# Kernel optimization log

Measured on AMD Instinct MI355X. Metric: run time of the kernel, lower is better.

The kernel has to match this reference:

```python
import jax, jax.numpy as jnp
import numpy as np


def _forward(f2e_emb, score_mat, rel_features, Wk, bk,
             batch_heads, batch_rels, batch_tails, edge_mat, eps):
    B, N, D = f2e_emb.shape
    R = rel_features.shape[0]
    dt = f2e_emb.dtype
    # -cdist(x, x) then row softmax (F.softmax dim=1 on a 2D mat == last axis)
    x2 = jnp.sum(f2e_emb * f2e_emb, axis=-1)                              # [B,N]
    d2 = x2[:, :, None] + x2[:, None, :] - 2.0 * jnp.einsum('bnd,bmd->bnm', f2e_emb, f2e_emb)
    sim = jax.nn.softmax(-jnp.sqrt(jnp.maximum(d2, 0.0)), axis=-1)        # [B,N,N]
    prob = jnp.einsum('bnk,bmk->bnm', sim, score_mat)                     # sim @ score_mat.T
    cand = (prob > eps) & (edge_mat < 1)                                  # candidate (row,col) pairs
    # torch.multinomial(sim[row], 1) per candidate pair -> gumbel-max categorical,
    # one independent draw per (b, row, col) over the row's similarity distribution
    logits = jnp.log(sim)[:, :, None, :]                                  # [B,N,1,N]
    s = jax.random.categorical(jax.random.key(42),
                               jax.lax.stop_gradient(jnp.broadcast_to(logits, (B, N, N, N))),
                               axis=-1)                                    # [B,N,N]
    b3 = jnp.arange(B)[:, None, None]
    r3 = jnp.arange(N)[None, :, None]
    c3 = jnp.arange(N)[None, None, :]
    new_rel = edge_mat[b3, s, c3]                                          # [B,N,N]
    valid = (cand & (new_rel != 0)).astype(dt)
    # per-(node, relation) incidence counts: exactly equivalent to the
    # fact2head_mat/fact2tail_mat sparse.mm aggregation of kb_self_linear(rel_features[rel])
    counts = jnp.zeros((B * N * R,), dt)
    counts = counts.at[((b3 * N + r3) * R + new_rel).ravel()].add(valid.ravel())  # new edge -> head
    counts = counts.at[((b3 * N + c3) * R + new_rel).ravel()].add(valid.ravel())  # new edge -> tail
    b2 = jnp.arange(B)[:, None]
    ones = jnp.ones(batch_heads.shape, dt)
    counts = counts.at[((b2 * N + batch_heads) * R + batch_rels).ravel()].add(ones.ravel())
    counts = counts.at[((b2 * N + batch_tails) * R + batch_rels).ravel()].add(ones.ravel())
    counts = counts.reshape(B, N, R)
    Wr = rel_features @ Wk + bk                                            # kb_self_linear(rel_features) [R,O]
    return jax.nn.relu(jnp.einsum('bnr,ro->bno', counts, Wr))              # [B,N,O]


def setup_inputs():
    key = jax.random.key(0)
    ks = jax.random.split(key, 10)
    B, N, D, O, R, E = 8, 256, 256, 256, 512, 8192
    return {
        'f2e_emb': jax.random.normal(ks[0], (B, N, D), jnp.float32),
        'score_mat': jax.random.normal(ks[1], (B, N, N), jnp.float32),
        'rel_features': jax.random.normal(ks[2], (R, D), jnp.float32),
        'Wk': jax.random.normal(ks[3], (D, O), jnp.float32) / np.sqrt(D).astype(np.float32),
        'bk': jnp.zeros((O,), jnp.float32),
        'local_entity': jax.random.randint(ks[4], (B, N), 0, N, jnp.int32),
        'batch_heads': jax.random.randint(ks[5], (B, E), 0, N, jnp.int32),
        'batch_rels': jax.random.randint(ks[6], (B, E), 0, R, jnp.int32),
        'batch_tails': jax.random.randint(ks[7], (B, E), 0, N, jnp.int32),
        'edge_mat': jax.random.randint(ks[8], (B, N, N), 0, 4, jnp.int32),
        'eps': 0,
    }


def reference(f2e_emb, score_mat, rel_features, Wk, bk, local_entity,
              batch_heads, batch_rels, batch_tails, edge_mat, eps):
    return _forward(f2e_emb, score_mat, rel_features, Wk, bk,
                    batch_heads, batch_rels, batch_tails, edge_mat, eps)
```

## Files before the change

kernel.cpp:

```cpp
#include <hip/hip_runtime.h>
#include <stdint.h>

#define B 8
#define N 256
#define D 256
#define O 256
#define R 512
#define E 8192
#define TRO 4
#define NSW 8192
#define F32_TINY 1.17549435e-38f

__device__ __forceinline__ void threefry2x32_k42(uint32_t x0, uint32_t x1,
                                                 uint32_t& o0, uint32_t& o1) {
  const uint32_t ks0 = 0u;
  const uint32_t ks1 = 42u;
  const uint32_t ks2 = 0u ^ 42u ^ 0x1BD11BDAu;
  x0 += ks0; x1 += ks1;
#define TF_R(r) { x0 += x1; x1 = (x1 << (r)) | (x1 >> (32 - (r))); x1 ^= x0; }
  TF_R(13) TF_R(15) TF_R(26) TF_R(6)
  x0 += ks1; x1 += ks2 + 1u;
  TF_R(17) TF_R(29) TF_R(16) TF_R(24)
  x0 += ks2; x1 += ks0 + 2u;
  TF_R(13) TF_R(15) TF_R(26) TF_R(6)
  x0 += ks0; x1 += ks1 + 3u;
  TF_R(17) TF_R(29) TF_R(16) TF_R(24)
  x0 += ks1; x1 += ks2 + 4u;
  TF_R(13) TF_R(15) TF_R(26) TF_R(6)
  x0 += ks2; x1 += ks0 + 5u;
#undef TF_R
  o0 = x0; o1 = x1;
}

__device__ __forceinline__ float gumbel_from_bits_f(float f) {
  float u = (f == 0.0f) ? F32_TINY : f;
  return -logf(-logf(u));
}

__global__ __launch_bounds__(256) void prep_kernel(const float* __restrict__ score,
                                                   float* __restrict__ scoreT,
                                                   const float* __restrict__ f2e,
                                                   float* __restrict__ f2eT,
                                                   const float* __restrict__ relf,
                                                   const float* __restrict__ Wk,
                                                   const float* __restrict__ bk,
                                                   float* __restrict__ Wr,
                                                   float* __restrict__ x2,
                                                   int* __restrict__ wcount) {
  int blk = blockIdx.x;
  int tid = threadIdx.x;
  if (blk == 0 && tid == 0) *wcount = 0;
  if (blk < 256) {
    __shared__ float tile[64][65];
    const float* src = (blk < 128) ? score : f2e;
    float* dst = (blk < 128) ? scoreT : f2eT;
    int b7 = blk & 127;
    int bb = b7 >> 4, t = b7 & 15, ti = t >> 2, tj = t & 3;
    size_t base = (size_t)bb * 65536;
    int c = tid & 63, r4 = tid >> 6;
#pragma unroll
    for (int rr = 0; rr < 64; rr += 4) {
      int row = rr + r4;
      tile[row][c] = src[base + (size_t)(ti * 64 + row) * 256 + tj * 64 + c];
    }
    __syncthreads();
#pragma unroll
    for (int rr = 0; rr < 64; rr += 4) {
      int row = rr + r4;
      dst[base + (size_t)(tj * 64 + row) * 256 + ti * 64 + c] = tile[c][row];
    }
  } else if (blk < 512) {
    __shared__ float rrow[2][D];
    int r0 = (blk - 256) * 2;
    int o = tid;
#pragma unroll
    for (int r = 0; r < 2; ++r) rrow[r][o] = relf[(size_t)(r0 + r) * D + o];
    __syncthreads();
    float aA0 = 0.f, aB0 = 0.f, aA1 = 0.f, aB1 = 0.f;
    for (int d = 0; d < D; d += 4) {
      float w0 = Wk[(size_t)(d + 0) * O + o];
      float w1 = Wk[(size_t)(d + 1) * O + o];
      float w2 = Wk[(size_t)(d + 2) * O + o];
      float w3 = Wk[(size_t)(d + 3) * O + o];
      float4 a0 = *(const float4*)&rrow[0][d];
      float4 a1 = *(const float4*)&rrow[1][d];
      aA0 += a0.x * w0; aB0 += a0.y * w1; aA0 += a0.z * w2; aB0 += a0.w * w3;
      aA1 += a1.x * w0; aB1 += a1.y * w1; aA1 += a1.z * w2; aB1 += a1.w * w3;
    }
    float bv = bk[o];
    Wr[(size_t)r0 * O + o] = (aA0 + aB0) + bv;
    Wr[(size_t)(r0 + 1) * O + o] = (aA1 + aB1) + bv;
  } else {
    int i = (blk - 512) * 256 + tid;
    const float4* p = (const float4*)(f2e + (size_t)i * D);
    double s = 0.0;
    for (int d = 0; d < D / 4; ++d) {
      float4 v = p[d];
      s += (double)v.x * v.x; s += (double)v.y * v.y;
      s += (double)v.z * v.z; s += (double)v.w * v.w;
    }
    x2[i] = (float)s;
  }
}

__global__ __launch_bounds__(256) void simcand_kernel(const float* __restrict__ f2e,
                                                      const float* __restrict__ f2eT,
                                                      const float* __restrict__ x2,
                                                      const float* __restrict__ scoreT,
                                                      const int* __restrict__ edge,
                                                      const int* __restrict__ epsp,
                                                      float* __restrict__ logits,
                                                      float* __restrict__ laux,
                                                      int* __restrict__ wlist,
                                                      int* __restrict__ wcount) {
  int bn0 = blockIdx.x * 2;
  int b = bn0 >> 8;
  int tid = threadIdx.x, lane = tid & 63, w = tid >> 6;
  __shared__ float arow[2][256];
  __shared__ float simrow[2][256];
  __shared__ float wred[2][4];
  __shared__ double dred[2][4];
  __shared__ float lnsh[2];
  arow[0][tid] = f2e[(size_t)bn0 * 256 + tid];
  arow[1][tid] = f2e[(size_t)(bn0 + 1) * 256 + tid];
  __syncthreads();
  float aA0 = 0.f, aB0 = 0.f, aA1 = 0.f, aB1 = 0.f;
  const float* fT = f2eT + (size_t)b * 65536 + tid;
  for (int dd = 0; dd < 256; dd += 4) {
    float b0 = fT[(size_t)(dd + 0) * 256];
    float b1 = fT[(size_t)(dd + 1) * 256];
    float b2 = fT[(size_t)(dd + 2) * 256];
    float b3 = fT[(size_t)(dd + 3) * 256];
    float4 a0 = *(const float4*)&arow[0][dd];
    float4 a1 = *(const float4*)&arow[1][dd];
    aA0 += a0.x * b0; aB0 += a0.y * b1; aA0 += a0.z * b2; aB0 += a0.w * b3;
    aA1 += a1.x * b0; aB1 += a1.y * b1; aA1 += a1.z * b2; aB1 += a1.w * b3;
  }
  float x2c = x2[b * 256 + tid];
  float neg0 = -sqrtf(fmaxf((x2[bn0] + x2c) - 2.0f * (aA0 + aB0), 0.0f));
  float neg1 = -sqrtf(fmaxf((x2[bn0 + 1] + x2c) - 2.0f * (aA1 + aB1), 0.0f));
  float m0 = neg0, m1 = neg1;
#pragma unroll
  for (int off = 32; off > 0; off >>= 1) {
    m0 = fmaxf(m0, __shfl_xor(m0, off));
    m1 = fmaxf(m1, __shfl_xor(m1, off));
  }
  if (lane == 0) { wred[0][w] = m0; wred[1][w] = m1; }
  __syncthreads();
  float mx0 = fmaxf(fmaxf(wred[0][0], wred[0][1]), fmaxf(wred[0][2], wred[0][3]));
  float mx1 = fmaxf(fmaxf(wred[1][0], wred[1][1]), fmaxf(wred[1][2], wred[1][3]));
  float p0 = expf(neg0 - mx0), p1 = expf(neg1 - mx1);
  double s0 = (double)p0, s1 = (double)p1;
#pragma unroll
  for (int off = 32; off > 0; off >>= 1) {
    s0 += __shfl_xor(s0, off);
    s1 += __shfl_xor(s1, off);
  }
  if (lane == 0) { dred[0][w] = s0; dred[1][w] = s1; }
  __syncthreads();
  float den0 = (float)(dred[0][0] + dred[0][1] + dred[0][2] + dred[0][3]);
  float den1 = (float)(dred[1][0] + dred[1][1] + dred[1][2] + dred[1][3]);
  float sv0 = p0 / den0, sv1 = p1 / den1;
  simrow[0][tid] = sv0; simrow[1][tid] = sv1;
  float l0 = logf(sv0), l1 = logf(sv1);
  logits[(size_t)bn0 * 256 + tid] = l0;
  logits[(size_t)(bn0 + 1) * 256 + tid] = l1;
  int d0 = bn0 & 255, d1 = (bn0 + 1) & 255;
  if (tid == d0) lnsh[0] = l0;
  if (tid == d1) lnsh[1] = l1;
  float e0 = (tid == d0) ? -3.4e38f : l0;
  float e1 = (tid == d1) ? -3.4e38f : l1;
#pragma unroll
  for (int off = 32; off > 0; off >>= 1) {
    e0 = fmaxf(e0, __shfl_xor(e0, off));
    e1 = fmaxf(e1, __shfl_xor(e1, off));
  }
  if (lane == 0) { wred[0][w] = e0; wred[1][w] = e1; }
  __syncthreads();
  if (tid == 0) {
    laux[2 * bn0 + 0] = lnsh[0];
    laux[2 * bn0 + 1] = fmaxf(fmaxf(wred[0][0], wred[0][1]), fmaxf(wred[0][2], wred[0][3]));
    laux[2 * bn0 + 2] = lnsh[1];
    laux[2 * bn0 + 3] = fmaxf(fmaxf(wred[1][0], wred[1][1]), fmaxf(wred[1][2], wred[1][3]));
  }
  float pA0 = 0.f, pB0 = 0.f, pA1 = 0.f, pB1 = 0.f;
  const float* sT = scoreT + (size_t)b * 65536 + tid;
  for (int kk = 0; kk < 256; kk += 4) {
    float b0 = sT[(size_t)(kk + 0) * 256];
    float b1 = sT[(size_t)(kk + 1) * 256];
    float b2 = sT[(size_t)(kk + 2) * 256];
    float b3 = sT[(size_t)(kk + 3) * 256];
    float4 q0 = *(const float4*)&simrow[0][kk];
    float4 q1 = *(const float4*)&simrow[1][kk];
    pA0 += q0.x * b0; pB0 += q0.y * b1; pA0 += q0.z * b2; pB0 += q0.w * b3;
    pA1 += q1.x * b0; pB1 += q1.y * b1; pA1 += q1.z * b2; pB1 += q1.w * b3;
  }
  float epsv = (float)epsp[0];
  float pr[2] = {pA0 + pB0, pA1 + pB1};
#pragma unroll
  for (int r = 0; r < 2; ++r) {
    int row = (bn0 + r) * 256 + tid;
    int em = edge[(size_t)row];
    bool active = (pr[r] > epsv) && (em < 1);
    unsigned long long mask = __ballot(active);
    int cnt = __popcll(mask);
    int basev = 0;
    if (lane == 0 && cnt) basev = atomicAdd(wcount, cnt);
    basev = __shfl(basev, 0);
    if (active) {
      int pos = basev + __popcll(mask & ((1ull << lane) - 1ull));
      wlist[pos] = row;
    }
  }
}

__global__ __launch_bounds__(256) void sample_kernel(const float* __restrict__ logits,
                                                     const float* __restrict__ laux,
                                                     const int* __restrict__ wlist,
                                                     const int* __restrict__ wcount,
                                                     const int* __restrict__ edge,
                                                     const int* __restrict__ heads,
                                                     const int* __restrict__ rels,
                                                     const int* __restrict__ tails,
                                                     float* __restrict__ counts) {
  int blk = blockIdx.x;
  if (blk >= 2048) {
    int i = (blk - 2048) * 256 + threadIdx.x;
    int b = i >> 13;
    int h = heads[i], r = rels[i], t = tails[i];
    atomicAdd(&counts[(size_t)(b * N + h) * R + r], 1.0f);
    atomicAdd(&counts[(size_t)(b * N + t) * R + r], 1.0f);
    return;
  }
  int lane = threadIdx.x & 63;
  int gw = blk * 4 + (threadIdx.x >> 6);
  int cnt = *wcount;
  for (int idx = gw; idx < cnt; idx += NSW) {
    int row = wlist[idx];
    int b = row >> 16;
    int n = (row >> 8) & 255;
    int c = row & 255;
    uint32_t base = (uint32_t)row << 8;
    float u0, u1, u2, u3;
    {
      uint32_t a0, a1;
#define GEN_U(q, dst)                                                     \
      threefry2x32_k42(0u, base + (uint32_t)((q) * 64 + lane), a0, a1);    \
      dst = __uint_as_float((((a0 ^ a1) >> 9)) | 0x3f800000u) - 1.0f;
      GEN_U(0, u0) GEN_U(1, u1) GEN_U(2, u2) GEN_U(3, u3)
#undef GEN_U
    }
    float l_n  = laux[2 * ((b << 8) + n) + 0];
    float Lmax = laux[2 * ((b << 8) + n) + 1];
    int qo = n >> 6;
    float uo = (qo == 0) ? u0 : (qo == 1) ? u1 : (qo == 2) ? u2 : u3;
    float u_n = __shfl(uo, n & 63);
    float v_n = gumbel_from_bits_f(u_n) + l_n;
    float thr_g = (v_n - Lmax) - 0.125f;
    float u_thr = expf(-expf(-thr_g));
    bool owner = (lane == (n & 63));
    bool anyc = ((u0 > u_thr) && !(owner && qo == 0)) |
                ((u1 > u_thr) && !(owner && qo == 1)) |
                ((u2 > u_thr) && !(owner && qo == 2)) |
                ((u3 > u_thr) && !(owner && qo == 3));
    if (!__any(anyc)) continue;

    const float* lrow = logits + (size_t)((b << 8) + n) * N;
    float bestv = -1e30f;
    int besti = 0;
    for (int q = 0; q < 4; ++q) {
      int k = q * 64 + lane;
      uint32_t o0, o1;
      threefry2x32_k42(0u, base + (uint32_t)k, o0, o1);
      uint32_t bits = o0 ^ o1;
      float f = __uint_as_float((bits >> 9) | 0x3f800000u) - 1.0f;
      float g = gumbel_from_bits_f(f);
      float v = g + lrow[k];
      if (v > bestv || (v == bestv && k < besti)) { bestv = v; besti = k; }
    }
    for (int off = 32; off > 0; off >>= 1) {
      float ov = __shfl_down(bestv, off);
      int oi = __shfl_down(besti, off);
      if (ov > bestv || (ov == bestv && oi < besti)) { bestv = ov; besti = oi; }
    }
    if (lane == 0) {
      int nr = edge[(size_t)((b << 8) + besti) * N + c];
      if (nr != 0) {
        atomicAdd(&counts[(size_t)((b << 8) + n) * R + nr], 1.0f);
        atomicAdd(&counts[(size_t)((b << 8) + c) * R + nr], 1.0f);
      }
    }
  }
}

__global__ __launch_bounds__(256) void out_kernel(const float* __restrict__ counts,
                                                  const float* __restrict__ Wr,
                                                  float* __restrict__ out) {
  int bn0 = blockIdx.x * TRO;
  int o = threadIdx.x;
  __shared__ float crow[TRO][R];
#pragma unroll
  for (int r = 0; r < TRO; ++r) {
    crow[r][o] = counts[(size_t)(bn0 + r) * R + o];
    crow[r][o + 256] = counts[(size_t)(bn0 + r) * R + 256 + o];
  }
  __syncthreads();
  float accA[TRO] = {0, 0, 0, 0}, accB[TRO] = {0, 0, 0, 0};
  for (int k = 0; k < R; k += 4) {
    float w0 = Wr[(size_t)(k + 0) * O + o];
    float w1 = Wr[(size_t)(k + 1) * O + o];
    float w2 = Wr[(size_t)(k + 2) * O + o];
    float w3 = Wr[(size_t)(k + 3) * O + o];
#pragma unroll
    for (int r = 0; r < TRO; ++r) {
      float4 cv = *(const float4*)&crow[r][k];
      accA[r] += cv.x * w0; accB[r] += cv.y * w1;
      accA[r] += cv.z * w2; accB[r] += cv.w * w3;
    }
  }
#pragma unroll
  for (int r = 0; r < TRO; ++r)
    out[(size_t)(bn0 + r) * O + o] = fmaxf(accA[r] + accB[r], 0.0f);
}

extern "C" void kernel_launch(void* const* d_in, const int* in_sizes, int n_in,
                              void* d_out, int out_size, void* d_ws, size_t ws_size,
                              hipStream_t stream) {
  (void)in_sizes; (void)n_in; (void)out_size; (void)ws_size;
  const float* f2e   = (const float*)d_in[0];
  const float* score = (const float*)d_in[1];
  const float* relf  = (const float*)d_in[2];
  const float* Wk    = (const float*)d_in[3];
  const float* bk    = (const float*)d_in[4];
  const int* heads   = (const int*)d_in[6];
  const int* rels    = (const int*)d_in[7];
  const int* tails   = (const int*)d_in[8];
  const int* edge    = (const int*)d_in[9];
  const int* epsp    = (const int*)d_in[10];
  float* out = (float*)d_out;

  float* ws     = (float*)d_ws;
  float* logits = ws;
  float* Wr     = logits + 524288;
  float* counts = Wr + 131072;
  float* scoreT = counts;
  float* f2eT   = counts + 524288;
  float* laux   = counts + 1048576;
  float* x2     = laux + 4096;
  int*   wlist  = (int*)(x2 + 2048);
  int*   wcount = wlist + 524288;

  prep_kernel<<<520, 256, 0, stream>>>(score, scoreT, f2e, f2eT,
                                       relf, Wk, bk, Wr, x2, wcount);
  simcand_kernel<<<(B * N) / 2, 256, 0, stream>>>(f2e, f2eT, x2, scoreT, edge, epsp,
                                                  logits, laux, wlist, wcount);
  hipMemsetAsync(counts, 0, (size_t)B * N * R * sizeof(float), stream);
  sample_kernel<<<2048 + 256, 256, 0, stream>>>(logits, laux, wlist, wcount, edge,
                                                heads, rels, tails, counts);
  out_kernel<<<(B * N) / TRO, 256, 0, stream>>>(counts, Wr, out);
}
```

Measured before the change: 204.8 us.

## Stage weight panels through LDS with register-prefetched float4 loads in matvec loops

Four matrix-vector style loops (Wr projection, distance GEMV, sim@score GEMV and the output counts@Wr product) used to read the B-operand one scalar per thread straight from global memory. They now load 16-row panels with float4 global loads into registers, write them to a shared buffer, and prefetch the next panel while computing on the current one. The goal is to widen memory transactions and hide global latency behind the arithmetic. In exchange each tile step adds two barriers and 16KB of extra LDS per block, which may reduce occupancy.

Measured after the change: 210.1 us. +2.6%, slower.

```diff
diff --git a/kernel.cpp b/kernel.cpp
--- a/kernel.cpp
+++ b/kernel.cpp
@@ -7,7 +7,6 @@
 #define O 256
 #define R 512
 #define E 8192
-#define TRO 4
 #define NSW 8192
 #define F32_TINY 1.17549435e-38f
 
@@ -36,6 +35,18 @@
   float u = (f == 0.0f) ? F32_TINY : f;
   return -logf(-logf(u));
 }
+
+#define LOADT(PANEL, KK)                                                      \
+  { const float* gp_ = (PANEL) + (size_t)((KK) * 16 + srow) * 256 + scol;     \
+    st0 = *(const float4*)gp_; gp_ += 1024;                                   \
+    st1 = *(const float4*)gp_; gp_ += 1024;                                   \
+    st2 = *(const float4*)gp_; gp_ += 1024;                                   \
+    st3 = *(const float4*)gp_; }
+#define WRITET()                                                              \
+  { *(float4*)&buf[srow][scol]      = st0;                                    \
+    *(float4*)&buf[srow + 4][scol]  = st1;                                    \
+    *(float4*)&buf[srow + 8][scol]  = st2;                                    \
+    *(float4*)&buf[srow + 12][scol] = st3; }
 
 __global__ __launch_bounds__(256) void prep_kernel(const float* __restrict__ score,
                                                    float* __restrict__ scoreT,
@@ -71,25 +82,33 @@
     }
   } else if (blk < 512) {
     __shared__ float rrow[2][D];
+    __shared__ float buf[16][256];
     int r0 = (blk - 256) * 2;
-    int o = tid;
-#pragma unroll
-    for (int r = 0; r < 2; ++r) rrow[r][o] = relf[(size_t)(r0 + r) * D + o];
-    __syncthreads();
+    int srow = tid >> 6, scol = (tid & 63) * 4;
+    float4 st0, st1, st2, st3;
+    rrow[0][tid] = relf[(size_t)r0 * D + tid];
+    rrow[1][tid] = relf[(size_t)(r0 + 1) * D + tid];
     float aA0 = 0.f, aB0 = 0.f, aA1 = 0.f, aB1 = 0.f;
-    for (int d = 0; d < D; d += 4) {
-      float w0 = Wk[(size_t)(d + 0) * O + o];
-      float w1 = Wk[(size_t)(d + 1) * O + o];
-      float w2 = Wk[(size_t)(d + 2) * O + o];
-      float w3 = Wk[(size_t)(d + 3) * O + o];
-      float4 a0 = *(const float4*)&rrow[0][d];
-      float4 a1 = *(const float4*)&rrow[1][d];
-      aA0 += a0.x * w0; aB0 += a0.y * w1; aA0 += a0.z * w2; aB0 += a0.w * w3;
-      aA1 += a1.x * w0; aB1 += a1.y * w1; aA1 += a1.z * w2; aB1 += a1.w * w3;
-    }
-    float bv = bk[o];
-    Wr[(size_t)r0 * O + o] = (aA0 + aB0) + bv;
-    Wr[(size_t)(r0 + 1) * O + o] = (aA1 + aB1) + bv;
+    LOADT(Wk, 0);
+    for (int kk = 0; kk < 16; ++kk) {
+      __syncthreads();
+      WRITET();
+      __syncthreads();
+      if (kk < 15) LOADT(Wk, kk + 1);
+      int dbase = kk * 16;
+#pragma unroll
+      for (int dd = 0; dd < 16; dd += 4) {
+        float4 a0 = *(const float4*)&rrow[0][dbase + dd];
+        float4 a1 = *(const float4*)&rrow[1][dbase + dd];
+        float b0 = buf[dd + 0][tid], b1 = buf[dd + 1][tid];
+        float b2 = buf[dd + 2][tid], b3 = buf[dd + 3][tid];
+        aA0 += a0.x * b0; aB0 += a0.y * b1; aA0 += a0.z * b2; aB0 += a0.w * b3;
+        aA1 += a1.x * b0; aB1 += a1.y * b1; aA1 += a1.z * b2; aB1 += a1.w * b3;
+      }
+    }
+    float bv = bk[tid];
+    Wr[(size_t)r0 * O + tid] = (aA0 + aB0) + bv;
+    Wr[(size_t)(r0 + 1) * O + tid] = (aA1 + aB1) + bv;
   } else {
     int i = (blk - 512) * 256 + tid;
     const float4* p = (const float4*)(f2e + (size_t)i * D);
@@ -118,24 +137,35 @@
   int tid = threadIdx.x, lane = tid & 63, w = tid >> 6;
   __shared__ float arow[2][256];
   __shared__ float simrow[2][256];
+  __shared__ float buf[16][256];
   __shared__ float wred[2][4];
   __shared__ double dred[2][4];
   __shared__ float lnsh[2];
+  int srow = tid >> 6, scol = (tid & 63) * 4;
+  float4 st0, st1, st2, st3;
   arow[0][tid] = f2e[(size_t)bn0 * 256 + tid];
   arow[1][tid] = f2e[(size_t)(bn0 + 1) * 256 + tid];
-  __syncthreads();
+  const float* panelF = f2eT + (size_t)b * 65536;
   float aA0 = 0.f, aB0 = 0.f, aA1 = 0.f, aB1 = 0.f;
-  const float* fT = f2eT + (size_t)b * 65536 + tid;
-  for (int dd = 0; dd < 256; dd += 4) {
-    float b0 = fT[(size_t)(dd + 0) * 256];
-    float b1 = fT[(size_t)(dd + 1) * 256];
-    float b2 = fT[(size_t)(dd + 2) * 256];
-    float b3 = fT[(size_t)(dd + 3) * 256];
-    float4 a0 = *(const float4*)&arow[0][dd];
-    float4 a1 = *(const float4*)&arow[1][dd];
-    aA0 += a0.x * b0; aB0 += a0.y * b1; aA0 += a0.z * b2; aB0 += a0.w * b3;
-    aA1 += a1.x * b0; aB1 += a1.y * b1; aA1 += a1.z * b2; aB1 += a1.w * b3;
-  }
+  LOADT(panelF, 0);
+  for (int kk = 0; kk < 16; ++kk) {
+    __syncthreads();
+    WRITET();
+    __syncthreads();
+    if (kk < 15) LOADT(panelF, kk + 1);
+    int dbase = kk * 16;
+#pragma unroll
+    for (int dd = 0; dd < 16; dd += 4) {
+      float4 a0 = *(const float4*)&arow[0][dbase + dd];
+      float4 a1 = *(const float4*)&arow[1][dbase + dd];
+      float b0 = buf[dd + 0][tid], b1 = buf[dd + 1][tid];
+      float b2 = buf[dd + 2][tid], b3 = buf[dd + 3][tid];
+      aA0 += a0.x * b0; aB0 += a0.y * b1; aA0 += a0.z * b2; aB0 += a0.w * b3;
+      aA1 += a1.x * b0; aB1 += a1.y * b1; aA1 += a1.z * b2; aB1 += a1.w * b3;
+    }
+  }
+  const float* panelS = scoreT + (size_t)b * 65536;
+  LOADT(panelS, 0);
   float x2c = x2[b * 256 + tid];
   float neg0 = -sqrtf(fmaxf((x2[bn0] + x2c) - 2.0f * (aA0 + aB0), 0.0f));
   float neg1 = -sqrtf(fmaxf((x2[bn0 + 1] + x2c) - 2.0f * (aA1 + aB1), 0.0f));
@@ -184,16 +214,21 @@
     laux[2 * bn0 + 3] = fmaxf(fmaxf(wred[1][0], wred[1][1]), fmaxf(wred[1][2], wred[1][3]));
   }
   float pA0 = 0.f, pB0 = 0.f, pA1 = 0.f, pB1 = 0.f;
-  const float* sT = scoreT + (size_t)b * 65536 + tid;
-  for (int kk = 0; kk < 256; kk += 4) {
-    float b0 = sT[(size_t)(kk + 0) * 256];
-    float b1 = sT[(size_t)(kk + 1) * 256];
-    float b2 = sT[(size_t)(kk + 2) * 256];
-    float b3 = sT[(size_t)(kk + 3) * 256];
-    float4 q0 = *(const float4*)&simrow[0][kk];
-    float4 q1 = *(const float4*)&simrow[1][kk];
-    pA0 += q0.x * b0; pB0 += q0.y * b1; pA0 += q0.z * b2; pB0 += q0.w * b3;
-    pA1 += q1.x * b0; pB1 += q1.y * b1; pA1 += q1.z * b2; pB1 += q1.w * b3;
+  for (int kk = 0; kk < 16; ++kk) {
+    __syncthreads();
+    WRITET();
+    __syncthreads();
+    if (kk < 15) LOADT(panelS, kk + 1);
+    int kbase = kk * 16;
+#pragma unroll
+    for (int dd = 0; dd < 16; dd += 4) {
+      float4 q0 = *(const float4*)&simrow[0][kbase + dd];
+      float4 q1 = *(const float4*)&simrow[1][kbase + dd];
+      float b0 = buf[dd + 0][tid], b1 = buf[dd + 1][tid];
+      float b2 = buf[dd + 2][tid], b3 = buf[dd + 3][tid];
+      pA0 += q0.x * b0; pB0 += q0.y * b1; pA0 += q0.z * b2; pB0 += q0.w * b3;
+      pA1 += q1.x * b0; pB1 += q1.y * b1; pA1 += q1.z * b2; pB1 += q1.w * b3;
+    }
   }
   float epsv = (float)epsp[0];
   float pr[2] = {pA0 + pB0, pA1 + pB1};
@@ -296,31 +331,41 @@
 __global__ __launch_bounds__(256) void out_kernel(const float* __restrict__ counts,
                                                   const float* __restrict__ Wr,
                                                   float* __restrict__ out) {
-  int bn0 = blockIdx.x * TRO;
-  int o = threadIdx.x;
-  __shared__ float crow[TRO][R];
-#pragma unroll
-  for (int r = 0; r < TRO; ++r) {
-    crow[r][o] = counts[(size_t)(bn0 + r) * R + o];
-    crow[r][o + 256] = counts[(size_t)(bn0 + r) * R + 256 + o];
-  }
-  __syncthreads();
-  float accA[TRO] = {0, 0, 0, 0}, accB[TRO] = {0, 0, 0, 0};
-  for (int k = 0; k < R; k += 4) {
-    float w0 = Wr[(size_t)(k + 0) * O + o];
-    float w1 = Wr[(size_t)(k + 1) * O + o];
-    float w2 = Wr[(size_t)(k + 2) * O + o];
-    float w3 = Wr[(size_t)(k + 3) * O + o];
-#pragma unroll
-    for (int r = 0; r < TRO; ++r) {
-      float4 cv = *(const float4*)&crow[r][k];
-      accA[r] += cv.x * w0; accB[r] += cv.y * w1;
-      accA[r] += cv.z * w2; accB[r] += cv.w * w3;
-    }
-  }
-#pragma unroll
-  for (int r = 0; r < TRO; ++r)
-    out[(size_t)(bn0 + r) * O + o] = fmaxf(accA[r] + accB[r], 0.0f);
+  int bn0 = blockIdx.x * 4;
+  int tid = threadIdx.x;
+  __shared__ float crow[4][512];
+  __shared__ float buf[16][256];
+  int srow = tid >> 6, scol = (tid & 63) * 4;
+  float4 st0, st1, st2, st3;
+  {
+    const float4* src = (const float4*)(counts + (size_t)bn0 * 512);
+    float* flat = &crow[0][0];
+    *(float4*)&flat[tid * 4] = src[tid];
+    *(float4*)&flat[1024 + tid * 4] = src[256 + tid];
+  }
+  float accA[4] = {0, 0, 0, 0}, accB[4] = {0, 0, 0, 0};
+  LOADT(Wr, 0);
+  for (int kk = 0; kk < 32; ++kk) {
+    __syncthreads();
+    WRITET();
+    __syncthreads();
+    if (kk < 31) LOADT(Wr, kk + 1);
+    int kbase = kk * 16;
+#pragma unroll
+    for (int dd = 0; dd < 16; dd += 4) {
+      float b0 = buf[dd + 0][tid], b1 = buf[dd + 1][tid];
+      float b2 = buf[dd + 2][tid], b3 = buf[dd + 3][tid];
+#pragma unroll
+      for (int r = 0; r < 4; ++r) {
+        float4 cv = *(const float4*)&crow[r][kbase + dd];
+        accA[r] += cv.x * b0; accB[r] += cv.y * b1;
+        accA[r] += cv.z * b2; accB[r] += cv.w * b3;
+      }
+    }
+  }
+#pragma unroll
+  for (int r = 0; r < 4; ++r)
+    out[(size_t)(bn0 + r) * O + tid] = fmaxf(accA[r] + accB[r], 0.0f);
 }
 
 extern "C" void kernel_launch(void* const* d_in, const int* in_sizes, int n_in,
@@ -357,5 +402,5 @@
   hipMemsetAsync(counts, 0, (size_t)B * N * R * sizeof(float), stream);
   sample_kernel<<<2048 + 256, 256, 0, stream>>>(logits, laux, wlist, wcount, edge,
                                                 heads, rels, tails, counts);
-  out_kernel<<<(B * N) / TRO, 256, 0, stream>>>(counts, Wr, out);
-}
+  out_kernel<<<(B * N) / 4, 256, 0, stream>>>(counts, Wr, out);
+}
```
